# Kernel optimization log

Measured on AMD Instinct MI355X. Metric: run time of the kernel, lower is better.

## Reference

```python
import jax, jax.numpy as jnp
import numpy as np

BLOCK_SIZES = [256] * 16
LAYER_SIZE = sum(BLOCK_SIZES)  # 4096
N_ROWS = 8192


def _block_diag_mask(sizes):
    m = np.zeros((sum(sizes), sum(sizes)), dtype=bool)
    off = 0
    for s in sizes:
        m[off:off + s, off:off + s] = True
        off += s
    return jnp.asarray(m)


def setup_inputs() -> dict:
    key = jax.random.key(0)
    k1, k2 = jax.random.split(key)
    mask = _block_diag_mask(BLOCK_SIZES)
    # _blocks param: block_diagonal(raw_blocks) -> dense matrix, zero off-block
    blocks = jax.random.normal(k1, (LAYER_SIZE, LAYER_SIZE), dtype=jnp.float32) * mask
    x = jax.random.normal(k2, (N_ROWS, LAYER_SIZE), dtype=jnp.float32)
    return {"x": x, "blocks": blocks, "mask": mask}


def reference(x, blocks, mask):
    # blocks property: mask then tanh (constrained='tanh'); tanh(0)=0 preserves structure
    b = jnp.tanh(blocks * mask)
    # forward: dense matmul x @ blocks (no bias)
    return x @ b
```

## Files before the change

kernel.cpp:

```cpp
#include <hip/hip_runtime.h>
#include <stdint.h>


typedef float floatx4 __attribute__((ext_vector_type(4)));
typedef __bf16 bf16x8 __attribute__((ext_vector_type(8)));

#define LDX 4096
#define NBLK 16
#define BS 256
#define WPJ 32
#define MSTEPS 16
#define MROWS 16

__device__ __forceinline__ unsigned int f2bf(float f) {
  union { float f; unsigned int i; } x;
  x.f = f;
  unsigned int r = x.i + 0x7FFFu + ((x.i >> 16) & 1u);
  return r >> 16;
}

__device__ __forceinline__ bf16x8 cvt8(float4 a, float4 b) {
  union { unsigned int u[4]; bf16x8 v; } r;
  r.u[0] = f2bf(a.x) | (f2bf(a.y) << 16);
  r.u[1] = f2bf(a.z) | (f2bf(a.w) << 16);
  r.u[2] = f2bf(b.x) | (f2bf(b.y) << 16);
  r.u[3] = f2bf(b.z) | (f2bf(b.w) << 16);
  return r.v;
}

__global__ __launch_bounds__(256) void tanh_pack(const float* __restrict__ blocks,
                                                 unsigned short* __restrict__ wsT) {
  __shared__ float tile[64][65];
  const int t = threadIdx.x;
  const int tc = blockIdx.x, tr = blockIdx.y, j = blockIdx.z;
  const float* src = blocks + (size_t)(j * BS + tr * 64) * LDX + j * BS + tc * 64;
#pragma unroll
  for (int it = 0; it < 8; ++it) {
    int v = it * 256 + t;
    int row = v >> 5;
    int c2 = (v & 31) * 2;
    float2 f = *(const float2*)(src + (size_t)row * LDX + c2);
    tile[row][c2] = tanhf(f.x);
    tile[row][c2 + 1] = tanhf(f.y);
  }
  __syncthreads();
  unsigned short* dst = wsT + (size_t)j * BS * BS + (size_t)(tc * 64) * BS + tr * 64;
#pragma unroll
  for (int it = 0; it < 8; ++it) {
    int v = it * 256 + t;
    int nn = v >> 5;
    int k2 = (v & 31) * 2;
    unsigned int pair = f2bf(tile[k2][nn]) | (f2bf(tile[k2 + 1][nn]) << 16);
    *(unsigned int*)(dst + (size_t)nn * BS + k2) = pair;
  }
}

__global__ __launch_bounds__(256, 2) void bdgemm_stream(const float* __restrict__ x,
                                                        const unsigned short* __restrict__ wsT,
                                                        float* __restrict__ out) {
  const int t = threadIdx.x;
  const int lane = t & 63;
  const int wave = t >> 6;
  const int mslab = blockIdx.x;
  const int j = blockIdx.y;
  const int fr = lane & 15;
  const int fq = (lane >> 4) * 8;
  const int n0w = wave * 64;
  const int r0 = (lane >> 4) * 4;

  const unsigned short* wb = wsT + (size_t)j * (BS * BS);
  bf16x8 Bf[8][4];
#pragma unroll
  for (int kw = 0; kw < 8; ++kw)
#pragma unroll
    for (int nf = 0; nf < 4; ++nf)
      Bf[kw][nf] = *(const bf16x8*)(wb + (size_t)(n0w + nf * 16 + fr) * BS + kw * 32 + fq);

  const int col0 = j * BS + n0w + fr;
  for (int step = 0; step < MSTEPS; ++step) {
    const int m0 = (mslab * MSTEPS + step) * MROWS;
    const float* ax = x + (size_t)(m0 + fr) * LDX + j * BS + fq;

    floatx4 acc[4];
#pragma unroll
    for (int nf = 0; nf < 4; ++nf) acc[nf] = (floatx4){0.f, 0.f, 0.f, 0.f};

#pragma unroll
    for (int kw = 0; kw < 8; ++kw) {
      float4 f0 = *(const float4*)(ax + kw * 32);
      float4 f1 = *(const float4*)(ax + kw * 32 + 4);
      bf16x8 av = cvt8(f0, f1);
#pragma unroll
      for (int nf = 0; nf < 4; ++nf)
        acc[nf] = __builtin_amdgcn_mfma_f32_16x16x32_bf16(av, Bf[kw][nf], acc[nf], 0, 0, 0);
    }

#pragma unroll
    for (int nf = 0; nf < 4; ++nf) {
      float* op = out + (size_t)(m0 + r0) * LDX + col0 + nf * 16;
#pragma unroll
      for (int r = 0; r < 4; ++r) op[(size_t)r * LDX] = acc[nf][r];
    }
  }
}

__global__ __launch_bounds__(256) void bdgemm_fused(const float* __restrict__ x,
                                                    const float* __restrict__ blocks,
                                                    float* __restrict__ out) {
  __shared__ unsigned short As[64 * 32];
  __shared__ unsigned short Bs[256 * 40];
  const int t = threadIdx.x;
  const int lane = t & 63;
  const int wave = t >> 6;
  const int mtile = blockIdx.x;
  const int j = blockIdx.y;
  const int m0 = mtile * 64;
  const float* xg = x + (size_t)m0 * LDX + j * BS;
  const int srow = t >> 2;
  const int scol = (t & 3) * 8;
  const int wn = wave * 64;
  const int fr = lane & 15;
  const int fq = (lane >> 4) * 8;

  floatx4 acc[4][4];
#pragma unroll
  for (int a = 0; a < 4; ++a)
#pragma unroll
    for (int b = 0; b < 4; ++b) acc[a][b] = (floatx4){0.f, 0.f, 0.f, 0.f};

  for (int kt = 0; kt < 8; ++kt) {
    const int k0 = kt * 32;
    const float* ap = xg + (size_t)srow * LDX + k0 + scol;
    float4 a0 = *(const float4*)(ap);
    float4 a1 = *(const float4*)(ap + 4);
    uint4 pk;
    pk.x = f2bf(a0.x) | (f2bf(a0.y) << 16);
    pk.y = f2bf(a0.z) | (f2bf(a0.w) << 16);
    pk.z = f2bf(a1.x) | (f2bf(a1.y) << 16);
    pk.w = f2bf(a1.z) | (f2bf(a1.w) << 16);
    *(uint4*)(As + t * 8) = pk;
#pragma unroll
    for (int i = 0; i < 32; ++i) {
      const int idx = i * 256 + t;
      const int kk = idx >> 8;
      const int nn = idx & 255;
      float v = tanhf(blocks[(size_t)(j * BS + k0 + kk) * LDX + j * BS + nn]);
      Bs[nn * 40 + kk] = (unsigned short)f2bf(v);
    }
    __syncthreads();
    bf16x8 af[4], bfm[4];
#pragma unroll
    for (int i = 0; i < 4; ++i) {
      af[i] = *(const bf16x8*)(As + (i * 16 + fr) * 32 + fq);
      bfm[i] = *(const bf16x8*)(Bs + (wn + i * 16 + fr) * 40 + fq);
    }
#pragma unroll
    for (int mi = 0; mi < 4; ++mi)
#pragma unroll
      for (int ni = 0; ni < 4; ++ni)
        acc[mi][ni] =
            __builtin_amdgcn_mfma_f32_16x16x32_bf16(af[mi], bfm[ni], acc[mi][ni], 0, 0, 0);
    __syncthreads();
  }
  const int r0 = (lane >> 4) * 4;
  const int ocol = j * BS + wn + fr;
#pragma unroll
  for (int mi = 0; mi < 4; ++mi)
#pragma unroll
    for (int ni = 0; ni < 4; ++ni) {
      float* op = out + (size_t)(m0 + mi * 16 + r0) * LDX + ocol + ni * 16;
#pragma unroll
      for (int r = 0; r < 4; ++r) op[(size_t)r * LDX] = acc[mi][ni][r];
    }
}

extern "C" void kernel_launch(void* const* d_in, const int* in_sizes, int n_in,
                              void* d_out, int out_size, void* d_ws, size_t ws_size,
                              hipStream_t stream) {
  const float* x = (const float*)d_in[0];
  const float* blocks = (const float*)d_in[1];
  float* out = (float*)d_out;

  const size_t need = (size_t)NBLK * BS * BS * sizeof(unsigned short);
  if (d_ws != nullptr && ws_size >= need) {
    unsigned short* wsT = (unsigned short*)d_ws;
    tanh_pack<<<dim3(4, 4, NBLK), 256, 0, stream>>>(blocks, wsT);
    bdgemm_stream<<<dim3(WPJ, NBLK), 256, 0, stream>>>(x, wsT, out);
  } else {
    bdgemm_fused<<<dim3(128, NBLK), 256, 0, stream>>>(x, blocks, out);
  }
}
```

Baseline: 357.5 us.

## Stream x rows into LDS with async triple-buffered global_load_lds pipeline

Replaces direct per-wave global loads of x in the streaming block-diagonal GEMM with a three-stage LDS ring buffer, filled by asynchronous global_load_lds copies issued up to three steps ahead. Each wave now loads a quarter of the 16x256 slab, so the four waves no longer each fetch the whole slab redundantly. Hand-coded waitcnt values and barriers order the copies against the LDS reads. This aims to hide HBM latency behind the MFMAs, in exchange for 48KB of LDS per block, extra barriers, and waitcnt encodings that must match the exact number of copies in flight.

```diff
diff --git a/kernel.cpp b/kernel.cpp
--- a/kernel.cpp
+++ b/kernel.cpp
@@ -10,7 +10,11 @@
 #define BS 256
 #define WPJ 32
 #define MSTEPS 16
-#define MROWS 16
+
+#define VMW8 0x0F78
+#define VMW24 0x4F78
+#define VMW40 0x8F78
+#define LGKM0 0xC07F
 
 __device__ __forceinline__ unsigned int f2bf(float f) {
   union { float f; unsigned int i; } x;
@@ -28,6 +32,13 @@
   return r.v;
 }
 
+__device__ __forceinline__ void async_copy16(const void* g, void* l) {
+  __builtin_amdgcn_global_load_lds(
+      (__attribute__((address_space(1))) void*)(uintptr_t)g,
+      (__attribute__((address_space(3))) void*)(unsigned int)(uintptr_t)l,
+      16, 0, 0);
+}
+
 __global__ __launch_bounds__(256) void tanh_pack(const float* __restrict__ blocks,
                                                  unsigned short* __restrict__ wsT) {
   __shared__ float tile[64][65];
@@ -55,18 +66,20 @@
   }
 }
 
-__global__ __launch_bounds__(256, 2) void bdgemm_stream(const float* __restrict__ x,
-                                                        const unsigned short* __restrict__ wsT,
-                                                        float* __restrict__ out) {
+__global__ __launch_bounds__(256, 2) void bdgemm_pipe(const float* __restrict__ x,
+                                                      const unsigned short* __restrict__ wsT,
+                                                      float* __restrict__ out) {
+  __shared__ float abuf[3][4096];
   const int t = threadIdx.x;
   const int lane = t & 63;
   const int wave = t >> 6;
   const int mslab = blockIdx.x;
   const int j = blockIdx.y;
   const int fr = lane & 15;
-  const int fq = (lane >> 4) * 8;
+  const int fqg = lane >> 4;
   const int n0w = wave * 64;
-  const int r0 = (lane >> 4) * 4;
+  const int r0 = fqg * 4;
+  const int mbase = mslab * (MSTEPS * 16);
 
   const unsigned short* wb = wsT + (size_t)j * (BS * BS);
   bf16x8 Bf[8][4];
@@ -74,27 +87,53 @@
   for (int kw = 0; kw < 8; ++kw)
 #pragma unroll
     for (int nf = 0; nf < 4; ++nf)
-      Bf[kw][nf] = *(const bf16x8*)(wb + (size_t)(n0w + nf * 16 + fr) * BS + kw * 32 + fq);
+      Bf[kw][nf] = *(const bf16x8*)(wb + (size_t)(n0w + nf * 16 + fr) * BS + kw * 32 + fqg * 8);
+
+  auto issue = [&](int s, int b) {
+    const float* g = x + (size_t)(mbase + s * 16 + fr) * LDX + j * BS;
+    char* l = (char*)&abuf[b][0];
+#pragma unroll
+    for (int q = 0; q < 4; ++q) {
+      const int kc = (wave * 4 + q) * 4 + fqg;
+      async_copy16(g + kc * 4, l + (wave * 4 + q) * 1024 + lane * 16);
+    }
+  };
+
+  issue(0, 0);
+  issue(1, 1);
+  issue(2, 2);
 
   const int col0 = j * BS + n0w + fr;
-  for (int step = 0; step < MSTEPS; ++step) {
-    const int m0 = (mslab * MSTEPS + step) * MROWS;
-    const float* ax = x + (size_t)(m0 + fr) * LDX + j * BS + fq;
+  for (int s = 0; s < MSTEPS; ++s) {
+    if (s == 0) __builtin_amdgcn_s_waitcnt(VMW8);
+    else if (s == 1) __builtin_amdgcn_s_waitcnt(VMW24);
+    else __builtin_amdgcn_s_waitcnt(VMW40);
+    __builtin_amdgcn_s_barrier();
+
+    const int b = s % 3;
+    const float* ab = &abuf[b][0];
+    bf16x8 av[8];
+#pragma unroll
+    for (int kw = 0; kw < 8; ++kw) {
+      const int kc0 = kw * 8 + fqg * 2;
+      float4 f0 = *(const float4*)(ab + kc0 * 64 + fr * 4);
+      float4 f1 = *(const float4*)(ab + (kc0 + 1) * 64 + fr * 4);
+      av[kw] = cvt8(f0, f1);
+    }
+    __builtin_amdgcn_s_waitcnt(LGKM0);
+    __builtin_amdgcn_s_barrier();
+    if (s + 3 < MSTEPS) issue(s + 3, b);
 
     floatx4 acc[4];
 #pragma unroll
     for (int nf = 0; nf < 4; ++nf) acc[nf] = (floatx4){0.f, 0.f, 0.f, 0.f};
-
-#pragma unroll
-    for (int kw = 0; kw < 8; ++kw) {
-      float4 f0 = *(const float4*)(ax + kw * 32);
-      float4 f1 = *(const float4*)(ax + kw * 32 + 4);
-      bf16x8 av = cvt8(f0, f1);
+#pragma unroll
+    for (int kw = 0; kw < 8; ++kw)
 #pragma unroll
       for (int nf = 0; nf < 4; ++nf)
-        acc[nf] = __builtin_amdgcn_mfma_f32_16x16x32_bf16(av, Bf[kw][nf], acc[nf], 0, 0, 0);
-    }
-
+        acc[nf] = __builtin_amdgcn_mfma_f32_16x16x32_bf16(av[kw], Bf[kw][nf], acc[nf], 0, 0, 0);
+
+    const int m0 = mbase + s * 16;
 #pragma unroll
     for (int nf = 0; nf < 4; ++nf) {
       float* op = out + (size_t)(m0 + r0) * LDX + col0 + nf * 16;
@@ -185,7 +224,7 @@
   if (d_ws != nullptr && ws_size >= need) {
     unsigned short* wsT = (unsigned short*)d_ws;
     tanh_pack<<<dim3(4, 4, NBLK), 256, 0, stream>>>(blocks, wsT);
-    bdgemm_stream<<<dim3(WPJ, NBLK), 256, 0, stream>>>(x, wsT, out);
+    bdgemm_pipe<<<dim3(WPJ, NBLK), 256, 0, stream>>>(x, wsT, out);
   } else {
     bdgemm_fused<<<dim3(128, NBLK), 256, 0, stream>>>(x, blocks, out);
   }
```

Result: faster. 326.4 us (-8.7%).

## Split K across waves with LDS reduction and prefetch next A tile

Applied to the files above, without the earlier changes.

Replaces the streaming kernel, in which each wave held the whole K range of B for its 64 output columns, with a split-K layout. Each of the four waves now covers a 64-wide K quarter for one 64-column N slab, and the partial sums are reduced through shared memory before a row-coalesced store. The grid grows by four times along N, B register use drops so the occupancy target rises to 4, and the next A rows are double-buffered in registers. In exchange it adds two barriers per step and LDS traffic, and each x element is now read by four blocks instead of one.

```diff
diff --git a/kernel.cpp b/kernel.cpp
--- a/kernel.cpp
+++ b/kernel.cpp
@@ -8,9 +8,8 @@
 #define LDX 4096
 #define NBLK 16
 #define BS 256
-#define WPJ 32
 #define MSTEPS 16
-#define MROWS 16
+#define CS 20
 
 __device__ __forceinline__ unsigned int f2bf(float f) {
   union { float f; unsigned int i; } x;
@@ -28,6 +27,10 @@
   return r.v;
 }
 
+__device__ __forceinline__ void lds_barrier() {
+  asm volatile("s_waitcnt lgkmcnt(0)\n\ts_barrier" ::: "memory");
+}
+
 __global__ __launch_bounds__(256) void tanh_pack(const float* __restrict__ blocks,
                                                  unsigned short* __restrict__ wsT) {
   __shared__ float tile[64][65];
@@ -55,52 +58,82 @@
   }
 }
 
-__global__ __launch_bounds__(256, 2) void bdgemm_stream(const float* __restrict__ x,
-                                                        const unsigned short* __restrict__ wsT,
-                                                        float* __restrict__ out) {
+__global__ __launch_bounds__(256, 4) void bdgemm_red(const float* __restrict__ x,
+                                                     const unsigned short* __restrict__ wsT,
+                                                     float* __restrict__ out) {
+  __shared__ float red[4 * 64 * CS];
   const int t = threadIdx.x;
   const int lane = t & 63;
-  const int wave = t >> 6;
-  const int mslab = blockIdx.x;
-  const int j = blockIdx.y;
+  const int w = t >> 6;
   const int fr = lane & 15;
-  const int fq = (lane >> 4) * 8;
-  const int n0w = wave * 64;
-  const int r0 = (lane >> 4) * 4;
+  const int q = lane >> 4;
+  const int nslab = blockIdx.x;
+  const int mslab = blockIdx.y;
+  const int j = blockIdx.z;
+  const int n0 = nslab * 64;
+  const int rowbase = mslab * (MSTEPS * 16);
 
   const unsigned short* wb = wsT + (size_t)j * (BS * BS);
-  bf16x8 Bf[8][4];
-#pragma unroll
-  for (int kw = 0; kw < 8; ++kw)
+  bf16x8 Bf[2][4];
+#pragma unroll
+  for (int kq = 0; kq < 2; ++kq)
 #pragma unroll
     for (int nf = 0; nf < 4; ++nf)
-      Bf[kw][nf] = *(const bf16x8*)(wb + (size_t)(n0w + nf * 16 + fr) * BS + kw * 32 + fq);
-
-  const int col0 = j * BS + n0w + fr;
-  for (int step = 0; step < MSTEPS; ++step) {
-    const int m0 = (mslab * MSTEPS + step) * MROWS;
-    const float* ax = x + (size_t)(m0 + fr) * LDX + j * BS + fq;
+      Bf[kq][nf] =
+          *(const bf16x8*)(wb + (size_t)(n0 + nf * 16 + fr) * BS + w * 64 + kq * 32 + q * 8);
+
+  const float* ax = x + (size_t)(rowbase + fr) * LDX + j * BS + w * 64 + q * 8;
+
+  float4 A[2][4];
+#pragma unroll
+  for (int kq = 0; kq < 2; ++kq) {
+    A[0][kq * 2] = *(const float4*)(ax + kq * 32);
+    A[0][kq * 2 + 1] = *(const float4*)(ax + kq * 32 + 4);
+  }
+
+  const int c = t & 63;
+  const int rq = t >> 6;
+  float* outb = out + (size_t)(rowbase + rq * 4) * LDX + j * BS + n0 + c;
+
+#pragma unroll
+  for (int s = 0; s < MSTEPS; ++s) {
+    const int p = s & 1;
+    if (s + 1 < MSTEPS) {
+      const float* an = ax + (size_t)(s + 1) * 16 * LDX;
+#pragma unroll
+      for (int kq = 0; kq < 2; ++kq) {
+        A[p ^ 1][kq * 2] = *(const float4*)(an + kq * 32);
+        A[p ^ 1][kq * 2 + 1] = *(const float4*)(an + kq * 32 + 4);
+      }
+    }
 
     floatx4 acc[4];
 #pragma unroll
     for (int nf = 0; nf < 4; ++nf) acc[nf] = (floatx4){0.f, 0.f, 0.f, 0.f};
-
-#pragma unroll
-    for (int kw = 0; kw < 8; ++kw) {
-      float4 f0 = *(const float4*)(ax + kw * 32);
-      float4 f1 = *(const float4*)(ax + kw * 32 + 4);
-      bf16x8 av = cvt8(f0, f1);
+#pragma unroll
+    for (int kq = 0; kq < 2; ++kq) {
+      bf16x8 av = cvt8(A[p][kq * 2], A[p][kq * 2 + 1]);
 #pragma unroll
       for (int nf = 0; nf < 4; ++nf)
-        acc[nf] = __builtin_amdgcn_mfma_f32_16x16x32_bf16(av, Bf[kw][nf], acc[nf], 0, 0, 0);
-    }
-
-#pragma unroll
-    for (int nf = 0; nf < 4; ++nf) {
-      float* op = out + (size_t)(m0 + r0) * LDX + col0 + nf * 16;
-#pragma unroll
-      for (int r = 0; r < 4; ++r) op[(size_t)r * LDX] = acc[nf][r];
-    }
+        acc[nf] = __builtin_amdgcn_mfma_f32_16x16x32_bf16(av, Bf[kq][nf], acc[nf], 0, 0, 0);
+    }
+
+#pragma unroll
+    for (int nf = 0; nf < 4; ++nf)
+      *(floatx4*)(&red[(w * 64 + nf * 16 + fr) * CS + q * 4]) = acc[nf];
+
+    lds_barrier();
+
+    floatx4 sum = *(const floatx4*)(&red[(0 * 64 + c) * CS + rq * 4]);
+#pragma unroll
+    for (int w2 = 1; w2 < 4; ++w2)
+      sum += *(const floatx4*)(&red[(w2 * 64 + c) * CS + rq * 4]);
+
+    float* op = outb + (size_t)s * 16 * LDX;
+#pragma unroll
+    for (int i = 0; i < 4; ++i) op[(size_t)i * LDX] = sum[i];
+
+    lds_barrier();
   }
 }
 
@@ -185,7 +218,7 @@
   if (d_ws != nullptr && ws_size >= need) {
     unsigned short* wsT = (unsigned short*)d_ws;
     tanh_pack<<<dim3(4, 4, NBLK), 256, 0, stream>>>(blocks, wsT);
-    bdgemm_stream<<<dim3(WPJ, NBLK), 256, 0, stream>>>(x, wsT, out);
+    bdgemm_red<<<dim3(4, 32, NBLK), 256, 0, stream>>>(x, wsT, out);
   } else {
     bdgemm_fused<<<dim3(128, NBLK), 256, 0, stream>>>(x, blocks, out);
   }
```

After: 401.1 us. +12.2%, slower.
